# Kernel optimization log

Hardware: AMD Instinct MI355X
Metric: run time of the kernel (lower is better)

## Reference

```python
import jax, jax.numpy as jnp
import numpy as np

N_HEAD = 16
D_HEAD = 64
D_MODEL = 1024
D_INNER = 4096
QLEN = 1024
MLEN = 1024
BSZ = 2
LN_EPS = 1e-5


def _layer_norm(x, g, b, eps=LN_EPS):
    mu = jnp.mean(x, axis=-1, keepdims=True)
    var = jnp.var(x, axis=-1, keepdims=True)
    return (x - mu) * jax.lax.rsqrt(var + eps) * g + b


def _rel_shift(x):
    # x: [qlen, rlen, bsz, n_head]
    q, r, b, n = x.shape
    zp = jnp.zeros((q, 1, b, n), x.dtype)
    xp = jnp.concatenate([zp, x], axis=1).reshape(r + 1, q, b, n)
    return xp[1:].reshape(q, r, b, n)


def setup_inputs() -> dict:
    key = jax.random.key(0)
    ks = jax.random.split(key, 12)
    klen = MLEN + QLEN
    w = jax.random.normal(ks[0], (QLEN, BSZ, D_MODEL), jnp.float32)
    r = jax.random.normal(ks[1], (klen, D_MODEL), jnp.float32)
    mems = jax.random.normal(ks[2], (MLEN, BSZ, D_MODEL), jnp.float32)
    # causal mask: query i attends keys j <= i + mlen
    i = jnp.arange(QLEN)[:, None]
    j = jnp.arange(klen)[None, :]
    attn_mask = (j > i + MLEN)[:, :, None]  # [qlen, klen, 1] bool
    s = 0.02
    params = dict(
        qkv_w=jax.random.normal(ks[3], (3 * N_HEAD * D_HEAD, D_MODEL), jnp.float32) * s,
        r_net_w=jax.random.normal(ks[4], (N_HEAD * D_HEAD, D_MODEL), jnp.float32) * s,
        o_w=jax.random.normal(ks[5], (D_MODEL, N_HEAD * D_HEAD), jnp.float32) * s,
        r_r_bias=jax.random.normal(ks[6], (N_HEAD, D_HEAD), jnp.float32) * s,
        r_w_bias=jax.random.normal(ks[7], (N_HEAD, D_HEAD), jnp.float32) * s,
        ln1_g=jnp.ones((D_MODEL,), jnp.float32),
        ln1_b=jnp.zeros((D_MODEL,), jnp.float32),
        ff_w1=jax.random.normal(ks[8], (D_INNER, D_MODEL), jnp.float32) * s,
        ff_b1=jnp.zeros((D_INNER,), jnp.float32),
        ff_w2=jax.random.normal(ks[9], (D_MODEL, D_INNER), jnp.float32) * s,
        ff_b2=jnp.zeros((D_MODEL,), jnp.float32),
        ln2_g=jnp.ones((D_MODEL,), jnp.float32),
        ln2_b=jnp.zeros((D_MODEL,), jnp.float32),
    )
    return dict(w=w, r=r, mems=mems, attn_mask=attn_mask, **params)


def reference(w, r, mems, attn_mask, qkv_w, r_net_w, o_w, r_r_bias, r_w_bias,
              ln1_g, ln1_b, ff_w1, ff_b1, ff_w2, ff_b2, ln2_g, ln2_b):
    qlen, bsz = w.shape[0], w.shape[1]
    scale = 1.0 / (D_HEAD ** 0.5)
    cat = jnp.concatenate([mems, w], axis=0)              # [klen, b, d_model]
    klen = cat.shape[0]
    w_heads = cat @ qkv_w.T                                # [klen, b, 3*n*d]
    wq, wk, wv = jnp.split(w_heads, 3, axis=-1)
    wq = wq[-qlen:]
    r_head_k = (r @ r_net_w.T).reshape(-1, N_HEAD, D_HEAD)  # [rlen, n, d]
    wq = wq.reshape(qlen, bsz, N_HEAD, D_HEAD)
    wk = wk.reshape(klen, bsz, N_HEAD, D_HEAD)
    wv = wv.reshape(klen, bsz, N_HEAD, D_HEAD)
    AC = jnp.einsum('ibnd,jbnd->ijbn', wq + r_w_bias, wk)   # content term
    BD = jnp.einsum('ibnd,jnd->ijbn', wq + r_r_bias, r_head_k)
    BD = _rel_shift(BD)                                     # position term
    attn_score = (AC + BD) * scale
    mask_value = jnp.finfo(attn_score.dtype).min
    attn_score = jnp.where(attn_mask[:, :, :, None], mask_value, attn_score)
    attn_prob = jax.nn.softmax(attn_score, axis=1)
    attn_vec = jnp.einsum('ijbn,jbnd->ibnd', attn_prob, wv)
    attn_vec = attn_vec.reshape(qlen, bsz, N_HEAD * D_HEAD)
    attn_out = attn_vec @ o_w.T
    h = _layer_norm(w + attn_out, ln1_g, ln1_b)             # post-lnorm
    core = jax.nn.relu(h @ ff_w1.T + ff_b1) @ ff_w2.T + ff_b2
    out = _layer_norm(h + core, ln2_g, ln2_b)
    return out
```

## Files before the change

kernel.cpp:

```cpp
#include <hip/hip_runtime.h>
#include <math.h>

#define QLEN 1024
#define MLEN 1024
#define KLEN 2048
#define BSZc 2
#define NH 16
#define DH 64
#define DM 1024
#define DI 4096

typedef unsigned short ushort_t;
typedef __attribute__((ext_vector_type(8))) short short8;
typedef __attribute__((ext_vector_type(4))) float f32x4;

__device__ __forceinline__ ushort_t f2bf(float x) {
    unsigned int u = __float_as_uint(x);
    unsigned int r = (u + 0x7FFFu + ((u >> 16) & 1u)) >> 16;
    return (ushort_t)r;
}

__device__ __forceinline__ void gload_lds16(const ushort_t* g, ushort_t* l) {
    __builtin_amdgcn_global_load_lds(
        (const __attribute__((address_space(1))) unsigned int*)g,
        (__attribute__((address_space(3))) unsigned int*)l,
        16, 0, 0);
}

__device__ __forceinline__ void cast8(const float* s, ushort_t* d, int g) {
    const float4 a = *(const float4*)(s + g * 8);
    const float4 b = *(const float4*)(s + g * 8 + 4);
    short8 o;
    o[0] = (short)f2bf(a.x); o[1] = (short)f2bf(a.y);
    o[2] = (short)f2bf(a.z); o[3] = (short)f2bf(a.w);
    o[4] = (short)f2bf(b.x); o[5] = (short)f2bf(b.y);
    o[6] = (short)f2bf(b.z); o[7] = (short)f2bf(b.w);
    *(short8*)(d + g * 8) = o;
}

__global__ __launch_bounds__(256)
void cast_phase1(const float* __restrict__ qkv_w, const float* __restrict__ rnet_w,
                 const float* __restrict__ mems, const float* __restrict__ w,
                 const float* __restrict__ r,
                 ushort_t* __restrict__ W1, ushort_t* __restrict__ W2,
                 ushort_t* __restrict__ Acat, ushort_t* __restrict__ Rsrc)
{
    int g = blockIdx.x * 256 + threadIdx.x;
    if (g < 393216)            { cast8(qkv_w,  W1,              g); }
    else if (g < 524288)       { cast8(rnet_w, W2,              g - 393216); }
    else if (g < 786432)       { cast8(mems,   Acat,            g - 524288); }
    else if (g < 1048576)      { cast8(w,      Acat + 2097152,  g - 786432); }
    else if (g < 1310720)      { cast8(r,      Rsrc,            g - 1048576); }
}

__global__ __launch_bounds__(256)
void cast_phase2(const float* __restrict__ o_w, const float* __restrict__ ffw1,
                 const float* __restrict__ ffw2,
                 ushort_t* __restrict__ W3, ushort_t* __restrict__ W4,
                 ushort_t* __restrict__ W5)
{
    int g = blockIdx.x * 256 + threadIdx.x;
    if (g < 131072)            { cast8(o_w,  W3, g); }
    else if (g < 655360)       { cast8(ffw1, W4, g - 131072); }
    else if (g < 1179648)      { cast8(ffw2, W5, g - 655360); }
}

template<int EMODE, int ACT, int BN, int SPLIT>
__global__ __launch_bounds__(256)
void gemm_mfma(const ushort_t* __restrict__ A, const ushort_t* __restrict__ B,
               const float* __restrict__ bias,
               void* __restrict__ O0v, void* __restrict__ O1v,
               int M, int N, int Ks, int lda, int ldb)
{
    constexpr int JT = BN / 32;
    __shared__ ushort_t At0[128 * 32];
    __shared__ ushort_t At1[128 * 32];
    __shared__ ushort_t Bt0[BN * 32];
    __shared__ ushort_t Bt1[BN * 32];

    const int tid  = threadIdx.x;
    const int lane = tid & 63;
    const int w    = tid >> 6;
    const int lr   = lane & 15;
    const int quad = lane >> 4;
    const int m0   = blockIdx.x * 128;
    const int n0   = blockIdx.y * BN;
    const int z    = (SPLIT > 1) ? (int)blockIdx.z : 0;
    const int kbase = z * Ks;
    const int wm0  = (w >> 1) * 64;
    const int wn0  = (w & 1) * (BN / 2);

    f32x4 acc[4][JT];
#pragma unroll
    for (int it = 0; it < 4; ++it)
#pragma unroll
        for (int jt = 0; jt < JT; ++jt) acc[it][jt] = (f32x4){0.f, 0.f, 0.f, 0.f};

    const int srow = lane >> 2;
    const int scol = (lane & 3) << 3;
    const ushort_t* Ag = A + (size_t)(m0 + w * 32 + srow) * lda + kbase + scol;
    ushort_t* a00 = At0 + (w * 32) * 32;
    ushort_t* a01 = At0 + (w * 32 + 16) * 32;
    ushort_t* a10 = At1 + (w * 32) * 32;
    ushort_t* a11 = At1 + (w * 32 + 16) * 32;
    const ushort_t* Bg;
    ushort_t *b00, *b01 = nullptr, *b10, *b11 = nullptr;
    if (BN == 128) {
        Bg  = B + (size_t)(n0 + w * 32 + srow) * ldb + kbase + scol;
        b00 = Bt0 + (w * 32) * 32;
        b01 = Bt0 + (w * 32 + 16) * 32;
        b10 = Bt1 + (w * 32) * 32;
        b11 = Bt1 + (w * 32 + 16) * 32;
    } else {
        Bg  = B + (size_t)(n0 + w * 16 + srow) * ldb + kbase + scol;
        b00 = Bt0 + (w * 16) * 32;
        b10 = Bt1 + (w * 16) * 32;
    }

    const ushort_t* Ato0 = At0 + (wm0 + lr) * 32 + quad * 8;
    const ushort_t* Ato1 = At1 + (wm0 + lr) * 32 + quad * 8;
    const ushort_t* Bto0 = Bt0 + (wn0 + lr) * 32 + quad * 8;
    const ushort_t* Bto1 = Bt1 + (wn0 + lr) * 32 + quad * 8;

    for (int k0 = 0; k0 < Ks; k0 += 64) {
        __syncthreads();
        gload_lds16(Ag + k0, a00);
        gload_lds16(Ag + (size_t)16 * lda + k0, a01);
        gload_lds16(Ag + k0 + 32, a10);
        gload_lds16(Ag + (size_t)16 * lda + k0 + 32, a11);
        if (BN == 128) {
            gload_lds16(Bg + k0, b00);
            gload_lds16(Bg + (size_t)16 * ldb + k0, b01);
            gload_lds16(Bg + k0 + 32, b10);
            gload_lds16(Bg + (size_t)16 * ldb + k0 + 32, b11);
        } else {
            gload_lds16(Bg + k0, b00);
            gload_lds16(Bg + k0 + 32, b10);
        }
        __syncthreads();

        short8 af[4], bf[JT];
#pragma unroll
        for (int it = 0; it < 4; ++it)
            af[it] = *(const short8*)(Ato0 + it * 16 * 32);
#pragma unroll
        for (int jt = 0; jt < JT; ++jt)
            bf[jt] = *(const short8*)(Bto0 + jt * 16 * 32);
#pragma unroll
        for (int it = 0; it < 4; ++it)
#pragma unroll
            for (int jt = 0; jt < JT; ++jt)
                acc[it][jt] = __builtin_amdgcn_mfma_f32_16x16x32_bf16(
                    af[it], bf[jt], acc[it][jt], 0, 0, 0);
#pragma unroll
        for (int it = 0; it < 4; ++it)
            af[it] = *(const short8*)(Ato1 + it * 16 * 32);
#pragma unroll
        for (int jt = 0; jt < JT; ++jt)
            bf[jt] = *(const short8*)(Bto1 + jt * 16 * 32);
#pragma unroll
        for (int it = 0; it < 4; ++it)
#pragma unroll
            for (int jt = 0; jt < JT; ++jt)
                acc[it][jt] = __builtin_amdgcn_mfma_f32_16x16x32_bf16(
                    af[it], bf[jt], acc[it][jt], 0, 0, 0);
    }

#pragma unroll
    for (int it = 0; it < 4; ++it)
#pragma unroll
        for (int jt = 0; jt < JT; ++jt)
#pragma unroll
            for (int rg = 0; rg < 4; ++rg) {
                const int m = m0 + wm0 + it * 16 + quad * 4 + rg;
                const int n = n0 + wn0 + jt * 16 + lr;
                float v = acc[it][jt][rg];
                if (EMODE == 0) {
                    float* dst = (float*)(z ? O1v : O0v);
                    if (bias && z == 0) v += bias[n];
                    dst[(size_t)m * N + n] = v;
                } else {
                    v += bias[n];
                    if (ACT == 1) v = fmaxf(v, 0.f);
                    ((ushort_t*)O0v)[(size_t)m * N + n] = f2bf(v);
                }
            }
}

__global__ __launch_bounds__(256)
void gemm_qkvr(const ushort_t* __restrict__ Acat, const ushort_t* __restrict__ W1,
               const ushort_t* __restrict__ Rsrc, const ushort_t* __restrict__ W2,
               ushort_t* __restrict__ Qac, ushort_t* __restrict__ Qbd,
               ushort_t* __restrict__ Kbf, ushort_t* __restrict__ Vtb,
               ushort_t* __restrict__ Rh,
               const float* __restrict__ rwb, const float* __restrict__ rrb)
{
    __shared__ ushort_t At0[128 * 32];
    __shared__ ushort_t At1[128 * 32];
    __shared__ ushort_t Bt0[128 * 32];
    __shared__ ushort_t Bt1[128 * 32];

    const int bid  = blockIdx.x;
    const bool isr = bid >= 768;
    const ushort_t* A; const ushort_t* B; int m0, n0;
    if (!isr) { A = Acat; B = W1; m0 = (bid & 31) * 128; n0 = (bid >> 5) * 128; }
    else { int t = bid - 768; A = Rsrc; B = W2; m0 = (t & 15) * 128; n0 = (t >> 4) * 128; }
    const int K = 1024;

    const int tid  = threadIdx.x;
    const int lane = tid & 63;
    const int w    = tid >> 6;
    const int lr   = lane & 15;
    const int quad = lane >> 4;
    const int wm0  = (w >> 1) * 64;
    const int wn0  = (w & 1) * 64;

    f32x4 acc[4][4];
#pragma unroll
    for (int it = 0; it < 4; ++it)
#pragma unroll
        for (int jt = 0; jt < 4; ++jt) acc[it][jt] = (f32x4){0.f, 0.f, 0.f, 0.f};

    const int srow = lane >> 2;
    const int scol = (lane & 3) << 3;
    const ushort_t* Ag = A + (size_t)(m0 + w * 32 + srow) * K + scol;
    const ushort_t* Bg = B + (size_t)(n0 + w * 32 + srow) * K + scol;
    ushort_t* a00 = At0 + (w * 32) * 32;
    ushort_t* a01 = At0 + (w * 32 + 16) * 32;
    ushort_t* a10 = At1 + (w * 32) * 32;
    ushort_t* a11 = At1 + (w * 32 + 16) * 32;
    ushort_t* b00 = Bt0 + (w * 32) * 32;
    ushort_t* b01 = Bt0 + (w * 32 + 16) * 32;
    ushort_t* b10 = Bt1 + (w * 32) * 32;
    ushort_t* b11 = Bt1 + (w * 32 + 16) * 32;

    const ushort_t* Ato0 = At0 + (wm0 + lr) * 32 + quad * 8;
    const ushort_t* Ato1 = At1 + (wm0 + lr) * 32 + quad * 8;
    const ushort_t* Bto0 = Bt0 + (wn0 + lr) * 32 + quad * 8;
    const ushort_t* Bto1 = Bt1 + (wn0 + lr) * 32 + quad * 8;

    for (int k0 = 0; k0 < K; k0 += 64) {
        __syncthreads();
        gload_lds16(Ag + k0, a00);
        gload_lds16(Ag + (size_t)16 * K + k0, a01);
        gload_lds16(Ag + k0 + 32, a10);
        gload_lds16(Ag + (size_t)16 * K + k0 + 32, a11);
        gload_lds16(Bg + k0, b00);
        gload_lds16(Bg + (size_t)16 * K + k0, b01);
        gload_lds16(Bg + k0 + 32, b10);
        gload_lds16(Bg + (size_t)16 * K + k0 + 32, b11);
        __syncthreads();

        short8 af[4], bf[4];
#pragma unroll
        for (int it = 0; it < 4; ++it)
            af[it] = *(const short8*)(Ato0 + it * 16 * 32);
#pragma unroll
        for (int jt = 0; jt < 4; ++jt)
            bf[jt] = *(const short8*)(Bto0 + jt * 16 * 32);
#pragma unroll
        for (int it = 0; it < 4; ++it)
#pragma unroll
            for (int jt = 0; jt < 4; ++jt)
                acc[it][jt] = __builtin_amdgcn_mfma_f32_16x16x32_bf16(
                    af[it], bf[jt], acc[it][jt], 0, 0, 0);
#pragma unroll
        for (int it = 0; it < 4; ++it)
            af[it] = *(const short8*)(Ato1 + it * 16 * 32);
#pragma unroll
        for (int jt = 0; jt < 4; ++jt)
            bf[jt] = *(const short8*)(Bto1 + jt * 16 * 32);
#pragma unroll
        for (int it = 0; it < 4; ++it)
#pragma unroll
            for (int jt = 0; jt < 4; ++jt)
                acc[it][jt] = __builtin_amdgcn_mfma_f32_16x16x32_bf16(
                    af[it], bf[jt], acc[it][jt], 0, 0, 0);
    }

#pragma unroll
    for (int it = 0; it < 4; ++it)
#pragma unroll
        for (int jt = 0; jt < 4; ++jt)
#pragma unroll
            for (int rg = 0; rg < 4; ++rg) {
                const int m = m0 + wm0 + it * 16 + quad * 4 + rg;
                const int n = n0 + wn0 + jt * 16 + lr;
                const float v = acc[it][jt][rg];
                if (!isr) {
                    const int j = m >> 1, b = m & 1;
                    const int part = n >> 10, hh = (n >> 6) & 15, d = n & 63;
                    if (part == 0) {
                        if (j >= MLEN) {
                            const int qi = j - MLEN;
                            const size_t qidx = (((size_t)(b * NH + hh)) * QLEN + qi) * DH + d;
                            Qac[qidx] = f2bf(v + rwb[hh * DH + d]);
                            Qbd[qidx] = f2bf(v + rrb[hh * DH + d]);
                        }
                    } else if (part == 1) {
                        Kbf[(((size_t)(b * NH + hh)) * KLEN + j) * DH + d] = f2bf(v);
                    } else {
                        Vtb[(((size_t)(b * NH + hh)) * DH + d) * KLEN + j] = f2bf(v);
                    }
                } else {
                    const int hh = n >> 6, d = n & 63;
                    Rh[(((size_t)hh) * KLEN + m) * DH + d] = f2bf(v);
                }
            }
}

__global__ __launch_bounds__(256, 3)
void attn_mfma(const ushort_t* __restrict__ Qac, const ushort_t* __restrict__ Qbd,
               const ushort_t* __restrict__ Kb, const ushort_t* __restrict__ Vt,
               const ushort_t* __restrict__ Rb,
               float* __restrict__ Op0, float* __restrict__ Op1,
               float* __restrict__ Mp, float* __restrict__ Lp)
{
    __shared__ __align__(16) ushort_t Kt[64 * 64];
    __shared__ __align__(16) ushort_t Rt[128 * 64];
    __shared__ __align__(16) ushort_t Vl[64 * 64];
    __shared__ __align__(16) float    Bw[4][16][84];

    const int tid  = threadIdx.x;
    const int lane = tid & 63;
    const int w    = tid >> 6;
    const int lr   = lane & 15;
    const int quad = lane >> 4;
    const int d    = blockIdx.x;
    const int L    = (d & 7) * 128 + (d >> 3);
    const int qt   = 15 - (L & 15);
    const int s    = (L >> 4) & 1;
    const int bh   = L >> 5;
    const int i0   = qt << 6;
    const int h    = bh & 15;
    const int b    = bh >> 4;

    short8 qaf[2], qbf[2];
    {
        const size_t rowoff = ((size_t)bh * QLEN + i0 + w * 16 + lr) * DH;
#pragma unroll
        for (int kt = 0; kt < 2; ++kt) {
            qaf[kt] = *(const short8*)(Qac + rowoff + kt * 32 + quad * 8);
            qbf[kt] = *(const short8*)(Qbd + rowoff + kt * 32 + quad * 8);
        }
    }

    f32x4 O[4];
#pragma unroll
    for (int nt = 0; nt < 4; ++nt) O[nt] = (f32x4){0.f, 0.f, 0.f, 0.f};
    float m_run = -3.4e38f, l_run = 0.f;

    const int nc   = qt + 17;
    const int half = (nc + 1) >> 1;
    const int c_lo = s ? half : 0;
    const int c_hi = s ? nc : half;
    const int stw  = 3 - w;
    const float SC = 0.125f * 1.44269504f;
    const ushort_t* Kh  = Kb + (size_t)bh * KLEN * DH;
    const ushort_t* Vh  = Vt + (size_t)bh * DH * KLEN;
    const ushort_t* Rhp = Rb + (size_t)h * KLEN * DH;

    const int lrow = lane >> 3;
    const int lsg  = lane & 7;
    const int sgo  = (lsg ^ lrow) << 3;
    const int xq   = lr & 7;
    const int fo0  = ((quad ^ xq)) << 3;
    const int fo1  = (((4 | quad) ^ xq)) << 3;

    {
        const int j0 = c_lo << 6;
        const int wb = 960 - i0 + j0;
#pragma unroll
        for (int t = 0; t < 2; ++t) {
            const int rb  = t * 32 + w * 8;
            gload_lds16(Kh + (size_t)(j0 + rb + lrow) * DH + sgo,
                        Kt + rb * 64);
        }
#pragma unroll
        for (int t = 0; t < 4; ++t) {
            const int gb = wb + t * 32 + w * 8;
            const int g  = gb + lrow;
            const int gc = g > (KLEN - 1) ? (KLEN - 1) : g;
            gload_lds16(Rhp + (size_t)gc * DH + sgo,
                        Rt + (gb & 127) * 64);
        }
    }

    for (int c = c_lo; c < c_hi; ++c) {
        const int j0 = c << 6;
        const int wb = 960 - i0 + j0;

        __syncthreads();

#pragma unroll
        for (int t = 0; t < 2; ++t) {
            const int db = t * 32 + w * 8;
            gload_lds16(Vh + (size_t)(db + lrow) * KLEN + j0 + sgo,
                        Vl + db * 64);
        }

#pragma unroll
        for (int ctl = 0; ctl < 5; ++ctl) {
            const int wr = (stw + ctl) * 16 + lr;
            const int ring = (wb + wr) & 127;
            f32x4 z = (f32x4){0.f, 0.f, 0.f, 0.f};
            short8 r0 = *(const short8*)&Rt[ring * 64 + fo0];
            z = __builtin_amdgcn_mfma_f32_16x16x32_bf16(qbf[0], r0, z, 0, 0, 0);
            short8 r1 = *(const short8*)&Rt[ring * 64 + fo1];
            z = __builtin_amdgcn_mfma_f32_16x16x32_bf16(qbf[1], r1, z, 0, 0, 0);
#pragma unroll
            for (int rg = 0; rg < 4; ++rg)
                Bw[w][quad * 4 + rg][ctl * 16 + lr] = z[rg];
        }
#pragma unroll
        for (int ct = 0; ct < 4; ++ct) {
            f32x4 z = (f32x4){0.f, 0.f, 0.f, 0.f};
            short8 k0f = *(const short8*)&Kt[(ct * 16 + lr) * 64 + fo0];
            z = __builtin_amdgcn_mfma_f32_16x16x32_bf16(qaf[0], k0f, z, 0, 0, 0);
            short8 k1f = *(const short8*)&Kt[(ct * 16 + lr) * 64 + fo1];
            z = __builtin_amdgcn_mfma_f32_16x16x32_bf16(qaf[1], k1f, z, 0, 0, 0);
#pragma unroll
            for (int rg = 0; rg < 4; ++rg) {
                const int rrow = quad * 4 + rg;
                Bw[w][rrow][ct * 16 + lr + 15 - rrow] += z[rg];
            }
        }

        const int lim = i0 + w * 16 + lr + 1024 - j0;
        float pv[16];
        float mx = -3.4e38f;
#pragma unroll
        for (int kt = 0; kt < 2; ++kt)
#pragma unroll
            for (int t = 0; t < 8; ++t) {
                const int jj = kt * 32 + quad * 8 + t;
                float sv = Bw[w][lr][jj + 15 - lr] * SC;
                sv = (jj > lim) ? -3.4e38f : sv;
                pv[kt * 8 + t] = sv;
                mx = fmaxf(mx, sv);
            }
        mx = fmaxf(mx, __shfl_xor(mx, 16, 64));
        mx = fmaxf(mx, __shfl_xor(mx, 32, 64));
        const float m_new = fmaxf(m_run, mx);
        float ps = 0.f;
        short8 pf[2];
#pragma unroll
        for (int kt = 0; kt < 2; ++kt)
#pragma unroll
            for (int t = 0; t < 8; ++t) {
                const float e = exp2f(pv[kt * 8 + t] - m_new);
                ps += e;
                pf[kt][t] = (short)f2bf(e);
            }
        ps += __shfl_xor(ps, 16, 64);
        ps += __shfl_xor(ps, 32, 64);
        const float alpha = exp2f(m_run - m_new);
        m_run = m_new;
        l_run = l_run * alpha + ps;

        __syncthreads();

        if (c + 1 < c_hi) {
            const int j1 = j0 + 64;
#pragma unroll
            for (int t = 0; t < 2; ++t) {
                const int rb = t * 32 + w * 8;
                gload_lds16(Kh + (size_t)(j1 + rb + lrow) * DH + sgo,
                            Kt + rb * 64);
            }
#pragma unroll
            for (int t = 0; t < 2; ++t) {
                const int gb = wb + 128 + t * 32 + w * 8;
                const int g  = gb + lrow;
                const int gc = g > (KLEN - 1) ? (KLEN - 1) : g;
                gload_lds16(Rhp + (size_t)gc * DH + sgo,
                            Rt + (gb & 127) * 64);
            }
        }

        float ar[4];
#pragma unroll
        for (int rg = 0; rg < 4; ++rg)
            ar[rg] = __shfl(alpha, quad * 4 + rg, 64);
#pragma unroll
        for (int nt = 0; nt < 4; ++nt) {
            O[nt][0] *= ar[0]; O[nt][1] *= ar[1];
            O[nt][2] *= ar[2]; O[nt][3] *= ar[3];
        }
        {
            short8 vb;
#pragma unroll
            for (int nt = 0; nt < 4; ++nt) {
                vb = *(const short8*)&Vl[(nt * 16 + lr) * 64 + fo0];
                O[nt] = __builtin_amdgcn_mfma_f32_16x16x32_bf16(pf[0], vb, O[nt], 0, 0, 0);
            }
#pragma unroll
            for (int nt = 0; nt < 4; ++nt) {
                vb = *(const short8*)&Vl[(nt * 16 + lr) * 64 + fo1];
                O[nt] = __builtin_amdgcn_mfma_f32_16x16x32_bf16(pf[1], vb, O[nt], 0, 0, 0);
            }
        }
    }

    if (quad == 0) {
        const size_t mi = ((size_t)s * 32 + bh) * QLEN + i0 + w * 16 + lr;
        Mp[mi] = m_run;
        Lp[mi] = l_run;
    }
    float* Op = s ? Op1 : Op0;
#pragma unroll
    for (int nt = 0; nt < 4; ++nt)
#pragma unroll
        for (int rg = 0; rg < 4; ++rg) {
            const int i = i0 + w * 16 + quad * 4 + rg;
            Op[((size_t)i * BSZc + b) * DM + h * DH + nt * 16 + lr] = O[nt][rg];
        }
}

__global__ __launch_bounds__(256)
void attn_merge(const float* __restrict__ O0, const float* __restrict__ O1,
                const float* __restrict__ Mp, const float* __restrict__ Lp,
                ushort_t* __restrict__ AV)
{
    const int row = blockIdx.x;
    const int tid = threadIdx.x;
    const int i = row >> 1, b = row & 1;
    const int h = tid >> 4;
    const int bh = b * NH + h;
    const size_t mi = (size_t)bh * QLEN + i;
    const float m1 = Mp[mi],             l1 = Lp[mi];
    const float m2 = Mp[32 * QLEN + mi], l2 = Lp[32 * QLEN + mi];
    const float M = fmaxf(m1, m2);
    const float a1 = exp2f(m1 - M), a2 = exp2f(m2 - M);
    const float rl = 1.f / (l1 * a1 + l2 * a2);
    const float f1 = a1 * rl, f2 = a2 * rl;
    const float4 o1 = ((const float4*)(O0 + (size_t)row * DM))[tid];
    const float4 o2 = ((const float4*)(O1 + (size_t)row * DM))[tid];
    ushort_t* p = AV + (size_t)row * DM + tid * 4;
    p[0] = f2bf(o1.x * f1 + o2.x * f2);
    p[1] = f2bf(o1.y * f1 + o2.y * f2);
    p[2] = f2bf(o1.z * f1 + o2.z * f2);
    p[3] = f2bf(o1.w * f1 + o2.w * f2);
}

__global__ __launch_bounds__(256)
void add_ln(const float* __restrict__ X, const float* __restrict__ Y0,
            const float* __restrict__ Y1,
            const float* __restrict__ gg, const float* __restrict__ bb,
            float* __restrict__ out, ushort_t* __restrict__ outb)
{
    const int row  = blockIdx.x;
    const int tid  = threadIdx.x;
    const int lane = tid & 63;
    const int w    = tid >> 6;
    __shared__ float ssum[4], ssq[4];

    const float4 xv = ((const float4*)(X + (size_t)row * DM))[tid];
    const float4 yv = ((const float4*)(Y0 + (size_t)row * DM))[tid];
    float v0 = xv.x + yv.x, v1 = xv.y + yv.y;
    float v2 = xv.z + yv.z, v3 = xv.w + yv.w;
    if (Y1) {
        const float4 zv = ((const float4*)(Y1 + (size_t)row * DM))[tid];
        v0 += zv.x; v1 += zv.y; v2 += zv.z; v3 += zv.w;
    }
    float s = v0 + v1 + v2 + v3;
    float q = v0 * v0 + v1 * v1 + v2 * v2 + v3 * v3;
#pragma unroll
    for (int off = 32; off > 0; off >>= 1) {
        s += __shfl_xor(s, off, 64);
        q += __shfl_xor(q, off, 64);
    }
    if (lane == 0) { ssum[w] = s; ssq[w] = q; }
    __syncthreads();
    s = ssum[0] + ssum[1] + ssum[2] + ssum[3];
    q = ssq[0] + ssq[1] + ssq[2] + ssq[3];
    const float mean = s * (1.f / DM);
    const float var  = q * (1.f / DM) - mean * mean;
    const float rs   = rsqrtf(var + 1e-5f);
    const float4 g4 = ((const float4*)gg)[tid];
    const float4 b4 = ((const float4*)bb)[tid];
    float4 ov;
    ov.x = (v0 - mean) * rs * g4.x + b4.x;
    ov.y = (v1 - mean) * rs * g4.y + b4.y;
    ov.z = (v2 - mean) * rs * g4.z + b4.z;
    ov.w = (v3 - mean) * rs * g4.w + b4.w;
    ((float4*)(out + (size_t)row * DM))[tid] = ov;
    if (outb) {
        ushort_t* p = outb + (size_t)row * DM + tid * 4;
        p[0] = f2bf(ov.x); p[1] = f2bf(ov.y);
        p[2] = f2bf(ov.z); p[3] = f2bf(ov.w);
    }
}

extern "C" void kernel_launch(void* const* d_in, const int* in_sizes, int n_in,
                              void* d_out, int out_size, void* d_ws, size_t ws_size,
                              hipStream_t stream)
{
    (void)in_sizes; (void)n_in; (void)out_size; (void)ws_size;
    const float* w      = (const float*)d_in[0];
    const float* r      = (const float*)d_in[1];
    const float* mems   = (const float*)d_in[2];
    const float* qkv_w  = (const float*)d_in[4];
    const float* rnet_w = (const float*)d_in[5];
    const float* o_w    = (const float*)d_in[6];
    const float* r_r_b  = (const float*)d_in[7];
    const float* r_w_b  = (const float*)d_in[8];
    const float* ln1g   = (const float*)d_in[9];
    const float* ln1b   = (const float*)d_in[10];
    const float* ffw1   = (const float*)d_in[11];
    const float* ffb1   = (const float*)d_in[12];
    const float* ffw2   = (const float*)d_in[13];
    const float* ffb2   = (const float*)d_in[14];
    const float* ln2g   = (const float*)d_in[15];
    const float* ln2b   = (const float*)d_in[16];
    float* out = (float*)d_out;

    char* wsb = (char*)d_ws;
    const size_t MB = 1024 * 1024;
    ushort_t* W1    = (ushort_t*)(wsb + 0 * MB);
    ushort_t* W2    = (ushort_t*)(wsb + 6 * MB);
    ushort_t* Acat  = (ushort_t*)(wsb + 8 * MB);
    ushort_t* Rsrc  = (ushort_t*)(wsb + 16 * MB);
    ushort_t* Qac   = (ushort_t*)(wsb + 20 * MB);
    ushort_t* Qbd   = (ushort_t*)(wsb + 24 * MB);
    ushort_t* Kbf   = (ushort_t*)(wsb + 28 * MB);
    ushort_t* Vt    = (ushort_t*)(wsb + 36 * MB);
    ushort_t* Rh    = (ushort_t*)(wsb + 44 * MB);
    float*    Op0   = (float*)(wsb + 48 * MB);
    float*    Op1   = (float*)(wsb + 56 * MB);
    float*    Mp    = (float*)(wsb + 4 * MB);
    float*    Lp    = (float*)(wsb + 4 * MB + 512 * 1024);
    ushort_t* AVec  = (ushort_t*)(wsb + 0 * MB);
    ushort_t* W3    = (ushort_t*)(wsb + 4 * MB);
    float*    AOut0 = (float*)(wsb + 8 * MB);
    float*    AOut1 = (float*)(wsb + 44 * MB);
    float*    Hbuf  = (float*)(wsb + 16 * MB);
    ushort_t* Hbf   = (ushort_t*)(wsb + 24 * MB);
    ushort_t* W4    = (ushort_t*)(wsb + 28 * MB);
    ushort_t* FFbf  = (ushort_t*)(wsb + 36 * MB);
    ushort_t* W5    = (ushort_t*)(wsb + 52 * MB);
    float*    Core0 = (float*)(wsb + 0 * MB);
    float*    Core1 = (float*)(wsb + 8 * MB);

    dim3 blk(256);

    cast_phase1<<<dim3(5120), blk, 0, stream>>>(qkv_w, rnet_w, mems, w, r,
                                                W1, W2, Acat, Rsrc);

    gemm_qkvr<<<dim3(896), blk, 0, stream>>>(
        Acat, W1, Rsrc, W2, Qac, Qbd, Kbf, Vt, Rh, r_w_b, r_r_b);

    attn_mfma<<<dim3(1024), blk, 0, stream>>>(
        Qac, Qbd, Kbf, Vt, Rh, Op0, Op1, Mp, Lp);

    attn_merge<<<dim3(2048), blk, 0, stream>>>(Op0, Op1, Mp, Lp, AVec);

    cast_phase2<<<dim3(4608), blk, 0, stream>>>(o_w, ffw1, ffw2, W3, W4, W5);

    gemm_mfma<0, 0, 64, 2><<<dim3(16, 16, 2), blk, 0, stream>>>(
        AVec, W3, nullptr, AOut0, AOut1, 2048, 1024, 512, 1024, 1024);

    add_ln<<<dim3(2 * QLEN), blk, 0, stream>>>(w, AOut0, AOut1, ln1g, ln1b, Hbuf, Hbf);

    gemm_mfma<3, 1, 128, 1><<<dim3(16, 32), blk, 0, stream>>>(
        Hbf, W4, ffb1, FFbf, nullptr, 2048, 4096, 1024, 1024, 1024);

    gemm_mfma<0, 0, 64, 2><<<dim3(16, 16, 2), blk, 0, stream>>>(
        FFbf, W5, ffb2, Core0, Core1, 2048, 1024, 2048, 4096, 4096);

    add_ln<<<dim3(2 * QLEN), blk, 0, stream>>>(Hbuf, Core0, Core1, ln2g, ln2b, out, nullptr);
}
```

Before: 384.3 us.

## Split attention KV range into 8-chunk segments with 3-4 way merge

The attention kernel previously split each query tile's key range into two halves. It now splits it into fixed 8-chunk segments, giving 4 segments for late query tiles and 3 for early ones, launched as 1792 blocks instead of 1024. The goal is shorter, more uniform blocks, which improves load balance and GPU fill. In exchange, the merge kernel has to read up to four partial outputs and their softmax statistics, which adds memory traffic. Workspace buffers are relocated to make room for the extra partials.

```diff
diff --git a/kernel.cpp b/kernel.cpp
--- a/kernel.cpp
+++ b/kernel.cpp
@@ -313,7 +313,7 @@
 void attn_mfma(const ushort_t* __restrict__ Qac, const ushort_t* __restrict__ Qbd,
                const ushort_t* __restrict__ Kb, const ushort_t* __restrict__ Vt,
                const ushort_t* __restrict__ Rb,
-               float* __restrict__ Op0, float* __restrict__ Op1,
+               float* __restrict__ OpA, float* __restrict__ OpB,
                float* __restrict__ Mp, float* __restrict__ Lp)
 {
     __shared__ __align__(16) ushort_t Kt[64 * 64];
@@ -327,10 +327,12 @@
     const int lr   = lane & 15;
     const int quad = lane >> 4;
     const int d    = blockIdx.x;
-    const int L    = (d & 7) * 128 + (d >> 3);
-    const int qt   = 15 - (L & 15);
-    const int s    = (L >> 4) & 1;
-    const int bh   = L >> 5;
+    const int L    = (d & 7) * 224 + (d >> 3);
+    const int bh   = L / 56;
+    const int r    = L % 56;
+    int qt, z;
+    if (r < 32) { qt = 15 - (r >> 2); z = r & 3; }
+    else        { int r2 = r - 32; int q3 = r2 / 3; qt = 7 - q3; z = r2 - q3 * 3; }
     const int i0   = qt << 6;
     const int h    = bh & 15;
     const int b    = bh >> 4;
@@ -351,9 +353,8 @@
     float m_run = -3.4e38f, l_run = 0.f;
 
     const int nc   = qt + 17;
-    const int half = (nc + 1) >> 1;
-    const int c_lo = s ? half : 0;
-    const int c_hi = s ? nc : half;
+    const int c_lo = z * 8;
+    const int c_hi = (c_lo + 8 < nc) ? (c_lo + 8) : nc;
     const int stw  = 3 - w;
     const float SC = 0.125f * 1.44269504f;
     const ushort_t* Kh  = Kb + (size_t)bh * KLEN * DH;
@@ -403,26 +404,26 @@
         for (int ctl = 0; ctl < 5; ++ctl) {
             const int wr = (stw + ctl) * 16 + lr;
             const int ring = (wb + wr) & 127;
-            f32x4 z = (f32x4){0.f, 0.f, 0.f, 0.f};
+            f32x4 zz = (f32x4){0.f, 0.f, 0.f, 0.f};
             short8 r0 = *(const short8*)&Rt[ring * 64 + fo0];
-            z = __builtin_amdgcn_mfma_f32_16x16x32_bf16(qbf[0], r0, z, 0, 0, 0);
+            zz = __builtin_amdgcn_mfma_f32_16x16x32_bf16(qbf[0], r0, zz, 0, 0, 0);
             short8 r1 = *(const short8*)&Rt[ring * 64 + fo1];
-            z = __builtin_amdgcn_mfma_f32_16x16x32_bf16(qbf[1], r1, z, 0, 0, 0);
+            zz = __builtin_amdgcn_mfma_f32_16x16x32_bf16(qbf[1], r1, zz, 0, 0, 0);
 #pragma unroll
             for (int rg = 0; rg < 4; ++rg)
-                Bw[w][quad * 4 + rg][ctl * 16 + lr] = z[rg];
+                Bw[w][quad * 4 + rg][ctl * 16 + lr] = zz[rg];
         }
 #pragma unroll
         for (int ct = 0; ct < 4; ++ct) {
-            f32x4 z = (f32x4){0.f, 0.f, 0.f, 0.f};
+            f32x4 zz = (f32x4){0.f, 0.f, 0.f, 0.f};
             short8 k0f = *(const short8*)&Kt[(ct * 16 + lr) * 64 + fo0];
-            z = __builtin_amdgcn_mfma_f32_16x16x32_bf16(qaf[0], k0f, z, 0, 0, 0);
+            zz = __builtin_amdgcn_mfma_f32_16x16x32_bf16(qaf[0], k0f, zz, 0, 0, 0);
             short8 k1f = *(const short8*)&Kt[(ct * 16 + lr) * 64 + fo1];
-            z = __builtin_amdgcn_mfma_f32_16x16x32_bf16(qaf[1], k1f, z, 0, 0, 0);
+            zz = __builtin_amdgcn_mfma_f32_16x16x32_bf16(qaf[1], k1f, zz, 0, 0, 0);
 #pragma unroll
             for (int rg = 0; rg < 4; ++rg) {
                 const int rrow = quad * 4 + rg;
-                Bw[w][rrow][ct * 16 + lr + 15 - rrow] += z[rg];
+                Bw[w][rrow][ct * 16 + lr + 15 - rrow] += zz[rg];
             }
         }
 
@@ -503,11 +504,12 @@
     }
 
     if (quad == 0) {
-        const size_t mi = ((size_t)s * 32 + bh) * QLEN + i0 + w * 16 + lr;
+        const size_t mi = ((size_t)(z * 32 + bh)) * QLEN + i0 + w * 16 + lr;
         Mp[mi] = m_run;
         Lp[mi] = l_run;
     }
-    float* Op = s ? Op1 : Op0;
+    float* Op = (z < 2) ? (OpA + (size_t)z * 2097152)
+                        : (OpB + (size_t)(z - 2) * 2097152);
 #pragma unroll
     for (int nt = 0; nt < 4; ++nt)
 #pragma unroll
@@ -518,7 +520,7 @@
 }
 
 __global__ __launch_bounds__(256)
-void attn_merge(const float* __restrict__ O0, const float* __restrict__ O1,
+void attn_merge(const float* __restrict__ OpA, const float* __restrict__ OpB,
                 const float* __restrict__ Mp, const float* __restrict__ Lp,
                 ushort_t* __restrict__ AV)
 {
@@ -528,19 +530,27 @@
     const int h = tid >> 4;
     const int bh = b * NH + h;
     const size_t mi = (size_t)bh * QLEN + i;
-    const float m1 = Mp[mi],             l1 = Lp[mi];
-    const float m2 = Mp[32 * QLEN + mi], l2 = Lp[32 * QLEN + mi];
-    const float M = fmaxf(m1, m2);
-    const float a1 = exp2f(m1 - M), a2 = exp2f(m2 - M);
-    const float rl = 1.f / (l1 * a1 + l2 * a2);
-    const float f1 = a1 * rl, f2 = a2 * rl;
-    const float4 o1 = ((const float4*)(O0 + (size_t)row * DM))[tid];
-    const float4 o2 = ((const float4*)(O1 + (size_t)row * DM))[tid];
+    const bool p4 = (i >= 512);
+    const float m0 = Mp[mi],                l0 = Lp[mi];
+    const float m1 = Mp[32 * QLEN + mi],    l1 = Lp[32 * QLEN + mi];
+    const float m2 = Mp[64 * QLEN + mi],    l2 = Lp[64 * QLEN + mi];
+    float m3 = -3.4e38f, l3 = 0.f;
+    if (p4) { m3 = Mp[96 * QLEN + mi]; l3 = Lp[96 * QLEN + mi]; }
+    const float M = fmaxf(fmaxf(m0, m1), fmaxf(m2, m3));
+    const float a0 = exp2f(m0 - M), a1 = exp2f(m1 - M);
+    const float a2 = exp2f(m2 - M), a3 = exp2f(m3 - M);
+    const float rl = 1.f / (l0 * a0 + l1 * a1 + l2 * a2 + l3 * a3);
+    const float f0 = a0 * rl, f1 = a1 * rl, f2 = a2 * rl, f3 = a3 * rl;
+    const float4 o0 = ((const float4*)(OpA + (size_t)row * DM))[tid];
+    const float4 o1 = ((const float4*)(OpA + 2097152 + (size_t)row * DM))[tid];
+    const float4 o2 = ((const float4*)(OpB + (size_t)row * DM))[tid];
+    float4 o3 = (float4){0.f, 0.f, 0.f, 0.f};
+    if (p4) o3 = ((const float4*)(OpB + 2097152 + (size_t)row * DM))[tid];
     ushort_t* p = AV + (size_t)row * DM + tid * 4;
-    p[0] = f2bf(o1.x * f1 + o2.x * f2);
-    p[1] = f2bf(o1.y * f1 + o2.y * f2);
-    p[2] = f2bf(o1.z * f1 + o2.z * f2);
-    p[3] = f2bf(o1.w * f1 + o2.w * f2);
+    p[0] = f2bf(o0.x * f0 + o1.x * f1 + o2.x * f2 + o3.x * f3);
+    p[1] = f2bf(o0.y * f0 + o1.y * f1 + o2.y * f2 + o3.y * f3);
+    p[2] = f2bf(o0.z * f0 + o1.z * f1 + o2.z * f2 + o3.z * f3);
+    p[3] = f2bf(o0.w * f0 + o1.w * f1 + o2.w * f2 + o3.w * f3);
 }
 
 __global__ __launch_bounds__(256)
@@ -626,11 +636,11 @@
     ushort_t* Kbf   = (ushort_t*)(wsb + 28 * MB);
     ushort_t* Vt    = (ushort_t*)(wsb + 36 * MB);
     ushort_t* Rh    = (ushort_t*)(wsb + 44 * MB);
-    float*    Op0   = (float*)(wsb + 48 * MB);
-    float*    Op1   = (float*)(wsb + 56 * MB);
-    float*    Mp    = (float*)(wsb + 4 * MB);
-    float*    Lp    = (float*)(wsb + 4 * MB + 512 * 1024);
-    ushort_t* AVec  = (ushort_t*)(wsb + 0 * MB);
+    float*    OpA   = (float*)(wsb + 0 * MB);
+    float*    OpB   = (float*)(wsb + 48 * MB);
+    float*    Mp    = (float*)(wsb + 16 * MB);
+    float*    Lp    = (float*)(wsb + 16 * MB + 512 * 1024);
+    ushort_t* AVec  = (ushort_t*)(wsb + 18 * MB);
     ushort_t* W3    = (ushort_t*)(wsb + 4 * MB);
     float*    AOut0 = (float*)(wsb + 8 * MB);
     float*    AOut1 = (float*)(wsb + 44 * MB);
@@ -650,10 +660,10 @@
     gemm_qkvr<<<dim3(896), blk, 0, stream>>>(
         Acat, W1, Rsrc, W2, Qac, Qbd, Kbf, Vt, Rh, r_w_b, r_r_b);
 
-    attn_mfma<<<dim3(1024), blk, 0, stream>>>(
-        Qac, Qbd, Kbf, Vt, Rh, Op0, Op1, Mp, Lp);
-
-    attn_merge<<<dim3(2048), blk, 0, stream>>>(Op0, Op1, Mp, Lp, AVec);
+    attn_mfma<<<dim3(1792), blk, 0, stream>>>(
+        Qac, Qbd, Kbf, Vt, Rh, OpA, OpB, Mp, Lp);
+
+    attn_merge<<<dim3(2048), blk, 0, stream>>>(OpA, OpB, Mp, Lp, AVec);
 
     cast_phase2<<<dim3(4608), blk, 0, stream>>>(o_w, ffw1, ffw2, W3, W4, W5);
 
```

New measurement: 385.6 us. Within noise of the previous version (+0.4%).
